# Performance work log

Measured on AMD Instinct MI355X. Metric: run time of the kernel, lower is better.

Reference implementation:

```python
import jax, jax.numpy as jnp
import numpy as np

T, B, E = 512, 128, 256  # timesteps, batch_size, embedding_size


def setup_inputs() -> dict:
    key = jax.random.key(0)
    k1, k2, k3 = jax.random.split(key, 3)
    return {
        "v": jax.random.normal(k1, (T, B, E), dtype=jnp.float32),
        "u": jax.random.uniform(k2, (T, B), dtype=jnp.float32),  # pop signals in (0,1)
        "d": jax.random.uniform(k3, (T, B), dtype=jnp.float32),  # push signals in (0,1)
    }


def _pop(s, w):
    """Grefenstette-stack pop: s [T,B] strengths (stack grows along dim 0,
    padded with zeros past the current depth), w [B] pop amount.
    Reverse cumsum, subtract w, clamp at 0, then difference to recover per-slot
    strengths. Zero padding at the tail is preserved exactly (contributes 0)."""
    top = jnp.cumsum(s[::-1], axis=0) - w[None, :]
    top = jnp.clip(top, 0.0)
    top = top - jnp.concatenate([jnp.zeros_like(top[:1]), top[:-1]], axis=0)
    return top[::-1]


def reference(v, u, d):
    # v: [T, B, E] pushed vectors; u, d: [T, B] pop/push strengths.
    T_, B_ = u.shape
    E_ = v.shape[-1]
    ones = jnp.ones((B_,), v.dtype)

    def step(carry, xs):
        V, s = carry  # V: [T,B,E] value buffer, s: [T,B] strengths (zero-padded)
        t, v_t, u_t, d_t = xs
        V = V.at[t].set(v_t)
        # forward(): pop with u (original detaches s and u inside pop), then push d
        s = _pop(jax.lax.stop_gradient(s), jax.lax.stop_gradient(u_t)).at[t].set(d_t)
        # read(): weights = s - pop(s, 1); r = sum_t weights * V
        weights = s - _pop(jax.lax.stop_gradient(s), ones)
        r = jnp.einsum('tb,tbe->be', weights, V)
        return (V, s), r

    init = (jnp.zeros((T_, B_, E_), v.dtype), jnp.zeros((T_, B_), v.dtype))
    _, rs = jax.lax.scan(step, init, (jnp.arange(T_), v, u, d))
    return rs  # [T, B, E] read vector at each timestep
```

## Files before the change

kernel.cpp:

```cpp
#include <hip/hip_runtime.h>

#define T_DIM 512
#define B_DIM 128
#define E_DIM 256
#define NEG_INF (-1e30f)

typedef float vfloat4 __attribute__((ext_vector_type(4)));


struct Node { float g; int ngl; };

__global__ void __launch_bounds__(512) scan_prep(
    const float* __restrict__ u, const float* __restrict__ d,
    float* __restrict__ S_out, Node* __restrict__ nodes)
{
    const int b    = blockIdx.x;
    const int t    = threadIdx.x;
    const int lane = t & 63;
    const int w    = t >> 6;

    __shared__ float wsum[8];
    __shared__ float wpre[8];
    __shared__ float M[10][T_DIM];

    const float dv = d[t * B_DIM + b];
    float x = dv - u[t * B_DIM + b];

    #pragma unroll
    for (int off = 1; off < 64; off <<= 1) {
        float y = __shfl_up(x, off, 64);
        if (lane >= off) x += y;
    }
    if (lane == 63) wsum[w] = x;
    __syncthreads();
    if (t < 8) {
        float s = 0.f;
        for (int i = 0; i < t; ++i) s += wsum[i];
        wpre[t] = s;
    }
    __syncthreads();
    const float S = x + wpre[w];
    const float g = dv - S;

    M[0][t] = g;
    __syncthreads();
    #pragma unroll
    for (int k = 1; k < 10; ++k) {
        int h = 1 << (k - 1);
        float left = (t >= h) ? M[k - 1][t - h] : NEG_INF;
        float mk = fmaxf(M[k - 1][t], left);
        __syncthreads();
        M[k][t] = mk;
        __syncthreads();
    }

    int m = t - 1;
    #pragma unroll
    for (int k = 9; k >= 0; --k) {
        if (m >= 0 && M[k][m] <= g) m -= (1 << k);
    }
    if (m < 0) m = -1;

    S_out[(b << 9) | t] = S;
    nodes[(b << 9) | t] = Node{g, m};
}

__global__ void __launch_bounds__(256) stack_read(
    const float* __restrict__ v, const float* __restrict__ S_in,
    const Node* __restrict__ nodes, float* __restrict__ out)
{
    const int bid  = blockIdx.x;
    const int swz  = ((bid & 7) << 10) | (bid >> 3);
    const int wid  = (swz << 2) | (threadIdx.x >> 6);
    const int lane = threadIdx.x & 63;
    const int id0  = wid << 1, id1 = id0 | 1;
    const int b0 = id0 >> 9, t0 = id0 & 511;
    const int b1 = id1 >> 9, t1 = id1 & 511;
    const int e4 = lane << 2;

    const float S0 = S_in[id0];
    const float S1 = S_in[id1];
    const Node* __restrict__ nb0 = nodes + (b0 << 9);
    const Node* __restrict__ nb1 = nodes + (b1 << 9);

    float4 acc0 = {0.f,0.f,0.f,0.f}, acc1 = {0.f,0.f,0.f,0.f};
    float prev0 = 0.f, prev1 = 0.f;
    int m0 = t0, m1 = t1;
    bool act0 = true, act1 = true;

    while (act0 || act1) {
        Node nd0, nd1; float4 vv0, vv1;
        if (act0) {
            nd0 = nb0[m0];
            vv0 = *(const float4*)(v + ((size_t)m0 * B_DIM + b0) * E_DIM + e4);
        }
        if (act1) {
            nd1 = nb1[m1];
            vv1 = *(const float4*)(v + ((size_t)m1 * B_DIM + b1) * E_DIM + e4);
        }
        if (act0) {
            float rc = S0 + nd0.g;
            float cur = fminf(rc, 1.f);
            float wt = cur - prev0;
            acc0.x += wt * vv0.x; acc0.y += wt * vv0.y;
            acc0.z += wt * vv0.z; acc0.w += wt * vv0.w;
            prev0 = cur;
            if (rc >= 1.f || nd0.ngl < 0) act0 = false; else m0 = nd0.ngl;
        }
        if (act1) {
            float rc = S1 + nd1.g;
            float cur = fminf(rc, 1.f);
            float wt = cur - prev1;
            acc1.x += wt * vv1.x; acc1.y += wt * vv1.y;
            acc1.z += wt * vv1.z; acc1.w += wt * vv1.w;
            prev1 = cur;
            if (rc >= 1.f || nd1.ngl < 0) act1 = false; else m1 = nd1.ngl;
        }
    }
    const vfloat4 o0 = {acc0.x, acc0.y, acc0.z, acc0.w};
    const vfloat4 o1 = {acc1.x, acc1.y, acc1.z, acc1.w};
    __builtin_nontemporal_store(o0,
        (vfloat4*)(out + ((size_t)t0 * B_DIM + b0) * E_DIM + e4));
    __builtin_nontemporal_store(o1,
        (vfloat4*)(out + ((size_t)t1 * B_DIM + b1) * E_DIM + e4));
}

extern "C" void kernel_launch(void* const* d_in, const int* in_sizes, int n_in,
                              void* d_out, int out_size, void* d_ws, size_t ws_size,
                              hipStream_t stream) {
    const float* v = (const float*)d_in[0];
    const float* u = (const float*)d_in[1];
    const float* d = (const float*)d_in[2];
    float* out = (float*)d_out;

    float* S    = (float*)d_ws;
    Node*  node = (Node*)((char*)d_ws + (size_t)B_DIM * T_DIM * 4);

    scan_prep<<<dim3(B_DIM), 512, 0, stream>>>(u, d, S, node);
    stack_read<<<dim3((T_DIM * B_DIM) / 8), 256, 0, stream>>>(v, S, node, out);
}
```

Before: 131.2 us.

## Stage node list in LDS and batch pointer-chasing to issue several v loads

Each block now holds 8 waves for a single batch row and first copies that row's node array (g, next-greater index) into shared memory. The pointer-chasing walk then reads from LDS instead of global memory. The walk is split into chunks of 8 steps: the chunk first resolves 8 indices and weights, then issues all 8 float4 loads of v per output before accumulating. This exposes memory-level parallelism that the old one-load-per-iteration dependent chain lacked, at the cost of more registers and some wasted loads of already-finished chains with zero weight.

```diff
diff --git a/kernel.cpp b/kernel.cpp
--- a/kernel.cpp
+++ b/kernel.cpp
@@ -4,6 +4,7 @@
 #define B_DIM 128
 #define E_DIM 256
 #define NEG_INF (-1e30f)
+#define NB 8
 
 typedef float vfloat4 __attribute__((ext_vector_type(4)));
 
@@ -65,23 +66,32 @@
     nodes[(b << 9) | t] = Node{g, m};
 }
 
-__global__ void __launch_bounds__(256) stack_read(
+__global__ void __launch_bounds__(512) stack_read(
     const float* __restrict__ v, const float* __restrict__ S_in,
     const Node* __restrict__ nodes, float* __restrict__ out)
 {
-    const int bid  = blockIdx.x;
-    const int swz  = ((bid & 7) << 10) | (bid >> 3);
-    const int wid  = (swz << 2) | (threadIdx.x >> 6);
+    __shared__ float2 snode[T_DIM];
+
+    const int bid = blockIdx.x;
+    const int swz = ((bid & 7) << 9) | (bid >> 3);
+    const int base_id = swz << 4;
+    const int b  = base_id >> 9;
+    const int wv = threadIdx.x >> 6;
     const int lane = threadIdx.x & 63;
-    const int id0  = wid << 1, id1 = id0 | 1;
-    const int b0 = id0 >> 9, t0 = id0 & 511;
-    const int b1 = id1 >> 9, t1 = id1 & 511;
     const int e4 = lane << 2;
 
+    {
+        const int i = threadIdx.x;
+        const Node nd = nodes[(b << 9) | i];
+        snode[i] = make_float2(nd.g, __int_as_float(nd.ngl));
+    }
+    __syncthreads();
+
+    const int id0 = base_id | (wv << 1), id1 = id0 | 1;
+    const int t0 = id0 & 511, t1 = id1 & 511;
     const float S0 = S_in[id0];
     const float S1 = S_in[id1];
-    const Node* __restrict__ nb0 = nodes + (b0 << 9);
-    const Node* __restrict__ nb1 = nodes + (b1 << 9);
+    const float* __restrict__ vb = v + (size_t)b * E_DIM + e4;
 
     float4 acc0 = {0.f,0.f,0.f,0.f}, acc1 = {0.f,0.f,0.f,0.f};
     float prev0 = 0.f, prev1 = 0.f;
@@ -89,40 +99,52 @@
     bool act0 = true, act1 = true;
 
     while (act0 || act1) {
-        Node nd0, nd1; float4 vv0, vv1;
-        if (act0) {
-            nd0 = nb0[m0];
-            vv0 = *(const float4*)(v + ((size_t)m0 * B_DIM + b0) * E_DIM + e4);
+        float wts0[NB], wts1[NB];
+        int   ms0[NB],  ms1[NB];
+
+        #pragma unroll
+        for (int k = 0; k < NB; ++k) {
+            if (act0) {
+                const float2 nd = snode[m0];
+                const float rc = S0 + nd.x;
+                const float cur = fminf(rc, 1.f);
+                wts0[k] = cur - prev0; prev0 = cur;
+                ms0[k] = m0;
+                const int ngl = __float_as_int(nd.y);
+                if (rc >= 1.f || ngl < 0) act0 = false; else m0 = ngl;
+            } else { wts0[k] = 0.f; ms0[k] = m0; }
+            if (act1) {
+                const float2 nd = snode[m1];
+                const float rc = S1 + nd.x;
+                const float cur = fminf(rc, 1.f);
+                wts1[k] = cur - prev1; prev1 = cur;
+                ms1[k] = m1;
+                const int ngl = __float_as_int(nd.y);
+                if (rc >= 1.f || ngl < 0) act1 = false; else m1 = ngl;
+            } else { wts1[k] = 0.f; ms1[k] = m1; }
         }
-        if (act1) {
-            nd1 = nb1[m1];
-            vv1 = *(const float4*)(v + ((size_t)m1 * B_DIM + b1) * E_DIM + e4);
+
+        float4 va0[NB], va1[NB];
+        #pragma unroll
+        for (int k = 0; k < NB; ++k) {
+            va0[k] = *(const float4*)(vb + ((size_t)ms0[k] << 15));
+            va1[k] = *(const float4*)(vb + ((size_t)ms1[k] << 15));
         }
-        if (act0) {
-            float rc = S0 + nd0.g;
-            float cur = fminf(rc, 1.f);
-            float wt = cur - prev0;
-            acc0.x += wt * vv0.x; acc0.y += wt * vv0.y;
-            acc0.z += wt * vv0.z; acc0.w += wt * vv0.w;
-            prev0 = cur;
-            if (rc >= 1.f || nd0.ngl < 0) act0 = false; else m0 = nd0.ngl;
-        }
-        if (act1) {
-            float rc = S1 + nd1.g;
-            float cur = fminf(rc, 1.f);
-            float wt = cur - prev1;
-            acc1.x += wt * vv1.x; acc1.y += wt * vv1.y;
-            acc1.z += wt * vv1.z; acc1.w += wt * vv1.w;
-            prev1 = cur;
-            if (rc >= 1.f || nd1.ngl < 0) act1 = false; else m1 = nd1.ngl;
+        #pragma unroll
+        for (int k = 0; k < NB; ++k) {
+            acc0.x += wts0[k] * va0[k].x; acc0.y += wts0[k] * va0[k].y;
+            acc0.z += wts0[k] * va0[k].z; acc0.w += wts0[k] * va0[k].w;
+            acc1.x += wts1[k] * va1[k].x; acc1.y += wts1[k] * va1[k].y;
+            acc1.z += wts1[k] * va1[k].z; acc1.w += wts1[k] * va1[k].w;
         }
     }
+
     const vfloat4 o0 = {acc0.x, acc0.y, acc0.z, acc0.w};
     const vfloat4 o1 = {acc1.x, acc1.y, acc1.z, acc1.w};
     __builtin_nontemporal_store(o0,
-        (vfloat4*)(out + ((size_t)t0 * B_DIM + b0) * E_DIM + e4));
+        (vfloat4*)(out + ((size_t)t0 * B_DIM + b) * E_DIM + e4));
     __builtin_nontemporal_store(o1,
-        (vfloat4*)(out + ((size_t)t1 * B_DIM + b1) * E_DIM + e4));
+        (vfloat4*)(out + ((size_t)t1 * B_DIM + b) * E_DIM + e4));
 }
 
 extern "C" void kernel_launch(void* const* d_in, const int* in_sizes, int n_in,
@@ -137,5 +159,5 @@
     Node*  node = (Node*)((char*)d_ws + (size_t)B_DIM * T_DIM * 4);
 
     scan_prep<<<dim3(B_DIM), 512, 0, stream>>>(u, d, S, node);
-    stack_read<<<dim3((T_DIM * B_DIM) / 8), 256, 0, stream>>>(v, S, node, out);
+    stack_read<<<dim3((T_DIM * B_DIM) / 16), 512, 0, stream>>>(v, S, node, out);
 }
```

New measurement: 138.2 us. 1.05x slower.
